# Kernel tuning notes

Hardware: AMD Instinct MI355X
Metric: run time of the kernel (lower is better)

Reference implementation:

```python
import jax, jax.numpy as jnp
import numpy as np

N_E, E_DIM, BETA = 8192, 512, 0.25


def setup_inputs() -> dict:
    key = jax.random.key(0)
    k1, k2 = jax.random.split(key)
    z = jax.random.normal(k1, (16, 1024, E_DIM), dtype=jnp.float32)
    # embedding initialized uniform(-1/n_e, 1/n_e)
    emb_w = jax.random.uniform(k2, (N_E, E_DIM), dtype=jnp.float32,
                               minval=-1.0 / N_E, maxval=1.0 / N_E)
    return {"z": z, "emb_w": emb_w}


def reference(z, emb_w):
    B, T, D = z.shape
    zf = z.reshape(-1, D)  # [BT, D]
    # squared-distance matrix: ||z||^2 + ||e||^2 - 2 z e^T  -> [BT, n_e]
    d = (jnp.sum(zf * zf, axis=1, keepdims=True)
         + jnp.sum(emb_w * emb_w, axis=1)
         - 2.0 * jnp.einsum('bd,nd->bn', zf, emb_w))
    idx = jnp.argmin(d, axis=1)  # [BT]
    z_q = emb_w[idx].reshape(z.shape)  # [B, T, D]
    # legacy=False: beta * commit + codebook term
    loss = (BETA * jnp.mean((jax.lax.stop_gradient(z_q) - z) ** 2)
            + jnp.mean((z_q - jax.lax.stop_gradient(z)) ** 2))
    # straight-through: value equals z_q
    z_q_st = z + jax.lax.stop_gradient(z_q - z)
    idx_out = idx.reshape(B, T)
    v = jnp.var(idx_out.astype(jnp.float32))
    return z_q_st, loss, idx_out, v
```

## Files before the change

kernel.cpp:

```cpp
#include <hip/hip_runtime.h>


#define BT   16384
#define DIMS 512
#define NE   8192
#define NS   4
#define BN   256
#define NTPB (NE / NS / BN)
#define NSTEPS 64

#define LOSS_OFF 8388608
#define IDX_OFF  8388609
#define V_OFF    8404993

#define BEST_OFF  0
#define ENORM_OFF 131072
#define SUMS_OFF  163840
#define CNT_OFF   163864

typedef __attribute__((ext_vector_type(8))) short short8;
typedef __attribute__((ext_vector_type(4))) float floatx4;

#define AS1(p) ((const __attribute__((address_space(1))) void*)(p))
#define AS3(p) ((__attribute__((address_space(3))) void*)(p))

__device__ __forceinline__ unsigned f2bf(float f) {
    unsigned u = __builtin_bit_cast(unsigned, f);
    u += 0x7FFFu + ((u >> 16) & 1u);
    return u >> 16;
}

__global__ __launch_bounds__(256) void prep_kernel(
    const float* __restrict__ z, const float* __restrict__ emb,
    ushort* __restrict__ zh, ushort* __restrict__ ehh,
    float* __restrict__ enorm, unsigned long long* __restrict__ best,
    double* __restrict__ sums, unsigned* __restrict__ counter)
{
    const int lane = threadIdx.x & 63, w = threadIdx.x >> 6;
    const int b = blockIdx.x;
    if (b < NE / 4) {
        const int row = b * 4 + w;
        const float4* p = (const float4*)(emb + (size_t)row * DIMS + lane * 8);
        float4 a = p[0], bb = p[1];
        uint4 h;
        h.x = f2bf(a.x) | (f2bf(a.y) << 16);
        h.y = f2bf(a.z) | (f2bf(a.w) << 16);
        h.z = f2bf(bb.x) | (f2bf(bb.y) << 16);
        h.w = f2bf(bb.z) | (f2bf(bb.w) << 16);
        *(uint4*)(ehh + (size_t)row * DIMS + lane * 8) = h;
        float s = a.x*a.x + a.y*a.y + a.z*a.z + a.w*a.w
                + bb.x*bb.x + bb.y*bb.y + bb.z*bb.z + bb.w*bb.w;
        #pragma unroll
        for (int off = 32; off > 0; off >>= 1) s += __shfl_down(s, off, 64);
        if (lane == 0) enorm[row] = s;
    } else {
        const int row = (b - NE / 4) * 4 + w;
        const float4* p = (const float4*)(z + (size_t)row * DIMS + lane * 8);
        float4 a = p[0], bb = p[1];
        uint4 h;
        h.x = f2bf(a.x) | (f2bf(a.y) << 16);
        h.y = f2bf(a.z) | (f2bf(a.w) << 16);
        h.z = f2bf(bb.x) | (f2bf(bb.y) << 16);
        h.w = f2bf(bb.z) | (f2bf(bb.w) << 16);
        *(uint4*)(zh + (size_t)row * DIMS + lane * 8) = h;
    }
    const int gid = b * 256 + threadIdx.x;
    if (gid < BT) best[gid] = 0xFFFFFFFFFFFFFFFFULL;
    if (gid == 0) { sums[0] = 0.0; sums[1] = 0.0; sums[2] = 0.0; *counter = 0u; }
}


__device__ __forceinline__ void dsr_fence() {
    asm volatile("s_waitcnt lgkmcnt(0)" ::: "memory");
    __builtin_amdgcn_sched_barrier(0);
}

#define DSR8(dst, IDX) do {                                                    \
    unsigned addr_ = (unsigned)(size_t)AS3(&lds[IDX]);                         \
    asm volatile("ds_read_b128 %0, %1" : "=v"(dst) : "v"(addr_));              \
} while (0)

#define LGK(N_) do {                                                           \
    asm volatile("s_waitcnt lgkmcnt(" #N_ ")" ::: "memory");                   \
    __builtin_amdgcn_sched_barrier(0);                                         \
} while (0)

#define CL4(J_, BIDX_, KK_)                                                    \
    _Pragma("unroll")                                                          \
    for (int mi = 0; mi < 4; mi++)                                             \
        acc[mi][J_] = __builtin_amdgcn_mfma_f32_16x16x32_bf16(                 \
            a[mi][KK_], b[BIDX_], acc[mi][J_], 0, 0, 0);

#define STAGE_A(SA_, H_) do {                                                  \
    const int sa_ = (SA_);                                                     \
    const int sc_ = sa_ & 63;                                                  \
    const unsigned al_ = (unsigned)(sa_ & 1) * 32768u                          \
                       + (unsigned)((((H_) * 128) + w * 8) * 64);              \
    const ushort* g_ = zA + (size_t)((H_) * 128) * DIMS + soff                 \
                     + ((sc_ & 7) * 64);                                       \
    __builtin_amdgcn_global_load_lds(AS1(g_), AS3(&lds[al_]), 16, 0, 0);       \
    __builtin_amdgcn_global_load_lds(AS1(g_ + (size_t)64 * DIMS),              \
                                     AS3(&lds[al_ + 64 * 64]), 16, 0, 0);      \
} while (0)

#define STAGE_B(SB_, H_) do {                                                  \
    const int sb_ = (SB_);                                                     \
    const int sc_ = sb_ & 63;                                                  \
    const unsigned bl_ = 16384u + (unsigned)(sb_ & 1) * 32768u                 \
                       + (unsigned)((((H_) * 128) + w * 8) * 64);              \
    const ushort* g_ = eh + (size_t)(nsN + (sc_ >> 3) * 256 + (H_) * 128) * DIMS \
                     + soff + ((sc_ & 7) * 64);                                \
    __builtin_amdgcn_global_load_lds(AS1(g_), AS3(&lds[bl_]), 16, 0, 0);       \
    __builtin_amdgcn_global_load_lds(AS1(g_ + (size_t)64 * DIMS),              \
                                     AS3(&lds[bl_ + 64 * 64]), 16, 0, 0);      \
} while (0)

#define STEP(S_, AB_, TM_) do {                                                \
    const int s_ = (S_);                                                       \
    short8 a[4][2], b[4];                                                      \
                                                                       \
    _Pragma("unroll") for (int mi = 0; mi < 4; mi++)                           \
        DSR8(a[mi][0], (AB_) + aro + mi * 1024 + pxo0);                        \
    _Pragma("unroll") for (int j = 0; j < 4; j++)                              \
        DSR8(b[j], 16384u + (AB_) + bro + j * 1024 + pxo0);                    \
    STAGE_B(s_ + 1, 0); STAGE_B(s_ + 1, 1);                                    \
    __builtin_amdgcn_s_setprio(1);                                             \
    LGK(3); CL4(0, 0, 0); LGK(2); CL4(1, 1, 0);                                \
    LGK(1); CL4(2, 2, 0); LGK(0); CL4(3, 3, 0);                                \
    __builtin_amdgcn_s_setprio(0);                                             \
                                                                       \
    _Pragma("unroll") for (int j = 0; j < 4; j++)                              \
        DSR8(b[j], 16384u + (AB_) + bro + (4 + j) * 1024 + pxo0);              \
    _Pragma("unroll") for (int mi = 0; mi < 4; mi++)                           \
        DSR8(a[mi][1], (AB_) + aro + mi * 1024 + pxo1);                        \
    STAGE_A(s_ + 1, 0); STAGE_A(s_ + 1, 1);                                    \
    __builtin_amdgcn_s_setprio(1);                                             \
    LGK(7); CL4(4, 0, 0); LGK(6); CL4(5, 1, 0);                                \
    LGK(5); CL4(6, 2, 0); LGK(4); CL4(7, 3, 0);                                \
    __builtin_amdgcn_s_setprio(0);                                             \
                                                                       \
    _Pragma("unroll") for (int j = 0; j < 4; j++)                              \
        DSR8(b[j], 16384u + (AB_) + bro + j * 1024 + pxo1);                    \
    __builtin_amdgcn_s_setprio(1);                                             \
    LGK(3); CL4(0, 0, 1); LGK(2); CL4(1, 1, 1);                                \
    LGK(1); CL4(2, 2, 1); LGK(0); CL4(3, 3, 1);                                \
    __builtin_amdgcn_s_setprio(0);                                             \
                                                                       \
    _Pragma("unroll") for (int j = 0; j < 4; j++)                              \
        DSR8(b[j], 16384u + (AB_) + bro + (4 + j) * 1024 + pxo1);              \
    __builtin_amdgcn_s_setprio(1);                                             \
    LGK(3); CL4(4, 0, 1); LGK(2); CL4(5, 1, 1);                                \
    LGK(1); CL4(6, 2, 1); LGK(0); CL4(7, 3, 1);                                \
    __builtin_amdgcn_s_setprio(0);                                             \
    __builtin_amdgcn_sched_barrier(0);                                         \
    if ((TM_) == 0) asm volatile("s_waitcnt vmcnt(0)" ::: "memory");           \
    __builtin_amdgcn_s_barrier();                                              \
} while (0)

__global__ __launch_bounds__(512, 2) void argmin_mfma(
    const ushort* __restrict__ zh, const ushort* __restrict__ eh,
    const float* __restrict__ enorm, unsigned long long* __restrict__ best)
{
    __shared__ __align__(16) ushort lds[69632];
    float* elds = (float*)&lds[65536];

    const int t = threadIdx.x;
    const int w = t >> 6, lane = t & 63;
    const int quad = lane >> 4, l15 = lane & 15;

    const int d = blockIdx.x;
    const int xcd = d & 7, slot = d >> 3;
    const int ns = xcd >> 1;
    const int mt = slot * 2 + (xcd & 1);
    const int m0 = mt * 256;
    const int nsN = ns * (NTPB * BN);

    const int wrow = (w & 3) * 64;
    const int wcol = (w >> 2) * 128;

    {
        float4 v = *(const float4*)(enorm + nsN + t * 4);
        *(float4*)(elds + t * 4) = v;
    }
    __syncthreads();

    const int l8 = lane >> 3, c8 = lane & 7;
    const int chunk = c8 ^ l8;
    const int soff = (w * 8 + l8) * DIMS + chunk * 8;
    const ushort* zA = zh + (size_t)m0 * DIMS;

    const int pxo0 = (quad ^ (l15 & 7)) * 8;
    const int pxo1 = ((4 + quad) ^ (l15 & 7)) * 8;
    const int aro = (wrow + l15) * 64;
    const int bro = (wcol + l15) * 64;

    floatx4 acc[4][8];
    #pragma unroll
    for (int mi = 0; mi < 4; mi++)
        #pragma unroll
        for (int nj = 0; nj < 8; nj++)
            acc[mi][nj] = (floatx4){0.f, 0.f, 0.f, 0.f};

    float bs[16];
    int   bn_[16];
    #pragma unroll
    for (int k = 0; k < 16; k++) { bs[k] = 3.4e38f; bn_[k] = 0; }

    STAGE_A(0, 0); STAGE_A(0, 1);
    STAGE_B(0, 0); STAGE_B(0, 1);
    asm volatile("s_waitcnt vmcnt(0)" ::: "memory");
    __builtin_amdgcn_s_barrier();

    for (int sp = 0; sp < NSTEPS; sp += 2) {
        STEP(sp, 0u, 0);
        STEP(sp + 1, 32768u, (sp == NSTEPS - 2) ? 2 : 0);

        if ((sp & 7) == 6) {
            const int nt = sp >> 3;
            const int eb = nt * 256 + wcol + l15;
            const int nbase = nsN + eb;
            float en[8];
            #pragma unroll
            for (int nj = 0; nj < 8; nj++) {
                unsigned addr_ = (unsigned)(size_t)AS3(&elds[eb + nj * 16]);
                asm volatile("ds_read_b32 %0, %1" : "=v"(en[nj]) : "v"(addr_));
            }
            dsr_fence();
            #pragma unroll
            for (int nj = 0; nj < 8; nj++) {
                const int n = nbase + nj * 16;
                #pragma unroll
                for (int mi = 0; mi < 4; mi++) {
                    #pragma unroll
                    for (int r = 0; r < 4; r++) {
                        const int k = mi * 4 + r;
                        const float sc = fmaf(-2.0f, acc[mi][nj][r], en[nj]);
                        if (sc < bs[k]) { bs[k] = sc; bn_[k] = n; }
                    }
                    acc[mi][nj] = (floatx4){0.f, 0.f, 0.f, 0.f};
                }
            }
        }
    }

    asm volatile("s_waitcnt vmcnt(0)" ::: "memory");

    #pragma unroll
    for (int mi = 0; mi < 4; mi++)
        #pragma unroll
        for (int r = 0; r < 4; r++) {
            const int k = mi * 4 + r;
            unsigned su = __builtin_bit_cast(unsigned, bs[k]);
            su = (su & 0x80000000u) ? ~su : (su | 0x80000000u);
            unsigned long long key = ((unsigned long long)su << 32) | (unsigned)bn_[k];
            #pragma unroll
            for (int off = 1; off < 16; off <<= 1) {
                unsigned long long o = __shfl_xor(key, off, 64);
                key = (o < key) ? o : key;
            }
            if (l15 == 0) atomicMin(&best[m0 + wrow + mi * 16 + quad * 4 + r], key);
        }
}

__global__ __launch_bounds__(256) void gather_loss_kernel(
    const float* __restrict__ z, const float* __restrict__ emb,
    const unsigned long long* __restrict__ best,
    float* __restrict__ out, double* __restrict__ sums, unsigned* __restrict__ counter)
{
    __shared__ int sIdx[32];
    __shared__ double red[4];
    const int t = threadIdx.x;
    const int row0 = blockIdx.x * 32;
    double myIdxSum = 0.0, myIdxSq = 0.0;
    if (t < 32) {
        int row = row0 + t;
        int idx = (int)(unsigned)(best[row] & 0xFFFFFFFFULL);
        sIdx[t] = idx;
        out[IDX_OFF + row] = (float)idx;
        myIdxSum = (double)idx;
        myIdxSq = (double)idx * (double)idx;
    }
    __syncthreads();
    double acc = 0.0;
    #pragma unroll 4
    for (int i = 0; i < 16; i++) {
        int e = i * 1024 + t * 4;
        int rl = e >> 9;
        int c = e & 511;
        int idx = sIdx[rl];
        float4 zv = *(const float4*)(z + (size_t)(row0 + rl) * DIMS + c);
        float4 ev = *(const float4*)(emb + (size_t)idx * DIMS + c);
        *(float4*)(out + (size_t)(row0 + rl) * DIMS + c) = ev;
        float dx = zv.x - ev.x, dy = zv.y - ev.y;
        float dz = zv.z - ev.z, dw = zv.w - ev.w;
        acc += (double)(dx * dx + dy * dy) + (double)(dz * dz + dw * dw);
    }
    const int lane = t & 63, wv = t >> 6;
    #pragma unroll
    for (int off = 32; off > 0; off >>= 1) {
        acc      += __shfl_down(acc, off, 64);
        myIdxSum += __shfl_down(myIdxSum, off, 64);
        myIdxSq  += __shfl_down(myIdxSq, off, 64);
    }
    if (lane == 0) red[wv] = acc;
    __syncthreads();
    if (t == 0) {
        double tot = red[0] + red[1] + red[2] + red[3];
        atomicAdd(&sums[0], tot);
        atomicAdd(&sums[1], myIdxSum);
        atomicAdd(&sums[2], myIdxSq);
        __threadfence();
        unsigned old = atomicAdd(counter, 1u);
        if (old == gridDim.x - 1) {
            __threadfence();
            double s0 = atomicAdd(&sums[0], 0.0);
            double s1 = atomicAdd(&sums[1], 0.0);
            double s2 = atomicAdd(&sums[2], 0.0);
            out[LOSS_OFF] = (float)(1.25 * s0 / (double)((size_t)BT * DIMS));
            double m = s1 / (double)BT;
            out[V_OFF] = (float)(s2 / (double)BT - m * m);
        }
    }
}

extern "C" void kernel_launch(void* const* d_in, const int* in_sizes, int n_in,
                              void* d_out, int out_size, void* d_ws, size_t ws_size,
                              hipStream_t stream) {
    const float* z = (const float*)d_in[0];
    const float* emb = (const float*)d_in[1];
    float* out = (float*)d_out;
    char* ws = (char*)d_ws;
    unsigned long long* best = (unsigned long long*)(ws + BEST_OFF);
    float* enorm  = (float*)(ws + ENORM_OFF);
    double* sums  = (double*)(ws + SUMS_OFF);
    unsigned* counter = (unsigned*)(ws + CNT_OFF);

    ushort* zh = (ushort*)out;
    ushort* ehh = zh + (size_t)BT * DIMS;

    hipLaunchKernelGGL(prep_kernel, dim3(NE / 4 + BT / 4), dim3(256), 0, stream,
                       z, emb, zh, ehh, enorm, best, sums, counter);
    hipLaunchKernelGGL(argmin_mfma, dim3(256), dim3(512), 0, stream,
                       zh, ehh, enorm, best);
    hipLaunchKernelGGL(gather_loss_kernel, dim3(BT / 32), dim3(256), 0, stream,
                       z, emb, best, out, sums, counter);
}
```

Measured before the change: 246.9 us.

## Triple-buffer A tiles in LDS and read codebook norms from global

The A (z) operand staging moves from a double buffer to a rotating triple buffer that is prefetched two steps ahead. The end-of-step wait becomes vmcnt(4) instead of vmcnt(0), so the newest A loads can stay in flight across the barrier. The LDS copy of enorm is dropped; norms are now loaded straight from global memory with inline global_load_dword followed by a full vmcnt(0) wait. The aim is to hide global-to-LDS latency better, at the cost of more LDS (which may cut occupancy below 2 blocks per CU) and a full drain of the memory queue at each argmin epilogue.

Result: slower. 253.5 us (+2.7%).

```diff
diff --git a/kernel.cpp b/kernel.cpp
--- a/kernel.cpp
+++ b/kernel.cpp
@@ -70,11 +70,6 @@
 }
 
 
-__device__ __forceinline__ void dsr_fence() {
-    asm volatile("s_waitcnt lgkmcnt(0)" ::: "memory");
-    __builtin_amdgcn_sched_barrier(0);
-}
-
 #define DSR8(dst, IDX) do {                                                    \
     unsigned addr_ = (unsigned)(size_t)AS3(&lds[IDX]);                         \
     asm volatile("ds_read_b128 %0, %1" : "=v"(dst) : "v"(addr_));              \
@@ -91,69 +86,65 @@
         acc[mi][J_] = __builtin_amdgcn_mfma_f32_16x16x32_bf16(                 \
             a[mi][KK_], b[BIDX_], acc[mi][J_], 0, 0, 0);
 
-#define STAGE_A(SA_, H_) do {                                                  \
-    const int sa_ = (SA_);                                                     \
-    const int sc_ = sa_ & 63;                                                  \
-    const unsigned al_ = (unsigned)(sa_ & 1) * 32768u                          \
-                       + (unsigned)((((H_) * 128) + w * 8) * 64);              \
+#define STAGE_A(SA_, H_, DST_) do {                                            \
+    const int sc_ = (SA_) & 63;                                                \
+    const unsigned al_ = (DST_) + (unsigned)((((H_) * 128) + w * 8) * 64);     \
     const ushort* g_ = zA + (size_t)((H_) * 128) * DIMS + soff                 \
                      + ((sc_ & 7) * 64);                                       \
     __builtin_amdgcn_global_load_lds(AS1(g_), AS3(&lds[al_]), 16, 0, 0);       \
     __builtin_amdgcn_global_load_lds(AS1(g_ + (size_t)64 * DIMS),              \
-                                     AS3(&lds[al_ + 64 * 64]), 16, 0, 0);      \
-} while (0)
-
-#define STAGE_B(SB_, H_) do {                                                  \
-    const int sb_ = (SB_);                                                     \
-    const int sc_ = sb_ & 63;                                                  \
-    const unsigned bl_ = 16384u + (unsigned)(sb_ & 1) * 32768u                 \
-                       + (unsigned)((((H_) * 128) + w * 8) * 64);              \
+                                     AS3(&lds[al_ + 4096]), 16, 0, 0);         \
+} while (0)
+
+#define STAGE_B(SB_, H_, DST_) do {                                            \
+    const int sc_ = (SB_) & 63;                                                \
+    const unsigned bl_ = (DST_) + (unsigned)((((H_) * 128) + w * 8) * 64);     \
     const ushort* g_ = eh + (size_t)(nsN + (sc_ >> 3) * 256 + (H_) * 128) * DIMS \
                      + soff + ((sc_ & 7) * 64);                                \
     __builtin_amdgcn_global_load_lds(AS1(g_), AS3(&lds[bl_]), 16, 0, 0);       \
     __builtin_amdgcn_global_load_lds(AS1(g_ + (size_t)64 * DIMS),              \
-                                     AS3(&lds[bl_ + 64 * 64]), 16, 0, 0);      \
-} while (0)
-
-#define STEP(S_, AB_, TM_) do {                                                \
+                                     AS3(&lds[bl_ + 4096]), 16, 0, 0);         \
+} while (0)
+
+#define STEP(S_, AR_, BR_, AW_, BW_, TM_) do {                                 \
     const int s_ = (S_);                                                       \
     short8 a[4][2], b[4];                                                      \
                                                                        \
     _Pragma("unroll") for (int mi = 0; mi < 4; mi++)                           \
-        DSR8(a[mi][0], (AB_) + aro + mi * 1024 + pxo0);                        \
+        DSR8(a[mi][0], (AR_) + aro + mi * 1024 + pxo0);                        \
     _Pragma("unroll") for (int j = 0; j < 4; j++)                              \
-        DSR8(b[j], 16384u + (AB_) + bro + j * 1024 + pxo0);                    \
-    STAGE_B(s_ + 1, 0); STAGE_B(s_ + 1, 1);                                    \
+        DSR8(b[j], (BR_) + bro + j * 1024 + pxo0);                             \
+    STAGE_B(s_ + 1, 0, BW_); STAGE_B(s_ + 1, 1, BW_);                          \
     __builtin_amdgcn_s_setprio(1);                                             \
     LGK(3); CL4(0, 0, 0); LGK(2); CL4(1, 1, 0);                                \
     LGK(1); CL4(2, 2, 0); LGK(0); CL4(3, 3, 0);                                \
     __builtin_amdgcn_s_setprio(0);                                             \
                                                                        \
     _Pragma("unroll") for (int j = 0; j < 4; j++)                              \
-        DSR8(b[j], 16384u + (AB_) + bro + (4 + j) * 1024 + pxo0);              \
+        DSR8(b[j], (BR_) + bro + (4 + j) * 1024 + pxo0);                       \
     _Pragma("unroll") for (int mi = 0; mi < 4; mi++)                           \
-        DSR8(a[mi][1], (AB_) + aro + mi * 1024 + pxo1);                        \
-    STAGE_A(s_ + 1, 0); STAGE_A(s_ + 1, 1);                                    \
+        DSR8(a[mi][1], (AR_) + aro + mi * 1024 + pxo1);                        \
+    STAGE_A(s_ + 2, 0, AW_); STAGE_A(s_ + 2, 1, AW_);                          \
     __builtin_amdgcn_s_setprio(1);                                             \
     LGK(7); CL4(4, 0, 0); LGK(6); CL4(5, 1, 0);                                \
     LGK(5); CL4(6, 2, 0); LGK(4); CL4(7, 3, 0);                                \
     __builtin_amdgcn_s_setprio(0);                                             \
                                                                        \
     _Pragma("unroll") for (int j = 0; j < 4; j++)                              \
-        DSR8(b[j], 16384u + (AB_) + bro + j * 1024 + pxo1);                    \
+        DSR8(b[j], (BR_) + bro + j * 1024 + pxo1);                             \
     __builtin_amdgcn_s_setprio(1);                                             \
     LGK(3); CL4(0, 0, 1); LGK(2); CL4(1, 1, 1);                                \
     LGK(1); CL4(2, 2, 1); LGK(0); CL4(3, 3, 1);                                \
     __builtin_amdgcn_s_setprio(0);                                             \
                                                                        \
     _Pragma("unroll") for (int j = 0; j < 4; j++)                              \
-        DSR8(b[j], 16384u + (AB_) + bro + (4 + j) * 1024 + pxo1);              \
+        DSR8(b[j], (BR_) + bro + (4 + j) * 1024 + pxo1);                       \
     __builtin_amdgcn_s_setprio(1);                                             \
     LGK(3); CL4(4, 0, 1); LGK(2); CL4(5, 1, 1);                                \
     LGK(1); CL4(6, 2, 1); LGK(0); CL4(7, 3, 1);                                \
     __builtin_amdgcn_s_setprio(0);                                             \
     __builtin_amdgcn_sched_barrier(0);                                         \
-    if ((TM_) == 0) asm volatile("s_waitcnt vmcnt(0)" ::: "memory");           \
+    if ((TM_) == 0) asm volatile("s_waitcnt vmcnt(4)" ::: "memory");           \
     __builtin_amdgcn_s_barrier();                                              \
 } while (0)
 
@@ -161,8 +152,7 @@
     const ushort* __restrict__ zh, const ushort* __restrict__ eh,
     const float* __restrict__ enorm, unsigned long long* __restrict__ best)
 {
-    __shared__ __align__(16) ushort lds[69632];
-    float* elds = (float*)&lds[65536];
+    __shared__ __align__(16) ushort lds[81920];
 
     const int t = threadIdx.x;
     const int w = t >> 6, lane = t & 63;
@@ -178,16 +168,11 @@
     const int wrow = (w & 3) * 64;
     const int wcol = (w >> 2) * 128;
 
-    {
-        float4 v = *(const float4*)(enorm + nsN + t * 4);
-        *(float4*)(elds + t * 4) = v;
-    }
-    __syncthreads();
-
     const int l8 = lane >> 3, c8 = lane & 7;
     const int chunk = c8 ^ l8;
     const int soff = (w * 8 + l8) * DIMS + chunk * 8;
     const ushort* zA = zh + (size_t)m0 * DIMS;
+    const float* enormg = enorm + nsN;
 
     const int pxo0 = (quad ^ (l15 & 7)) * 8;
     const int pxo1 = ((4 + quad) ^ (l15 & 7)) * 8;
@@ -206,14 +191,19 @@
     #pragma unroll
     for (int k = 0; k < 16; k++) { bs[k] = 3.4e38f; bn_[k] = 0; }
 
-    STAGE_A(0, 0); STAGE_A(0, 1);
-    STAGE_B(0, 0); STAGE_B(0, 1);
-    asm volatile("s_waitcnt vmcnt(0)" ::: "memory");
+    STAGE_A(0, 0, 0u);     STAGE_A(0, 1, 0u);
+    STAGE_B(0, 0, 49152u); STAGE_B(0, 1, 49152u);
+    STAGE_A(1, 0, 16384u); STAGE_A(1, 1, 16384u);
+    asm volatile("s_waitcnt vmcnt(4)" ::: "memory");
     __builtin_amdgcn_s_barrier();
 
+    unsigned aR = 0u, aN = 16384u, aW = 32768u;
+
     for (int sp = 0; sp < NSTEPS; sp += 2) {
-        STEP(sp, 0u, 0);
-        STEP(sp + 1, 32768u, (sp == NSTEPS - 2) ? 2 : 0);
+        STEP(sp, aR, 49152u, aW, 65536u, 0);
+        { unsigned t_ = aR; aR = aN; aN = aW; aW = t_; }
+        STEP(sp + 1, aR, 65536u, aW, 49152u, (sp == NSTEPS - 2) ? 2 : 0);
+        { unsigned t_ = aR; aR = aN; aN = aW; aW = t_; }
 
         if ((sp & 7) == 6) {
             const int nt = sp >> 3;
@@ -222,10 +212,12 @@
             float en[8];
             #pragma unroll
             for (int nj = 0; nj < 8; nj++) {
-                unsigned addr_ = (unsigned)(size_t)AS3(&elds[eb + nj * 16]);
-                asm volatile("ds_read_b32 %0, %1" : "=v"(en[nj]) : "v"(addr_));
+                const float* ep_ = enormg + eb + nj * 16;
+                asm volatile("global_load_dword %0, %1, off"
+                             : "=v"(en[nj]) : "v"(ep_));
             }
-            dsr_fence();
+            asm volatile("s_waitcnt vmcnt(0)" ::: "memory");
+            __builtin_amdgcn_sched_barrier(0);
             #pragma unroll
             for (int nj = 0; nj < 8; nj++) {
                 const int n = nbase + nj * 16;
```
